# Kernel tuning notes

Hardware: AMD Instinct MI355X
Metric: run time of the kernel (lower is better)

## Reference

```python
import jax, jax.numpy as jnp
import numpy as np

D_MODEL = 512
N_HEADS = 8
D_HEAD = D_MODEL // N_HEADS
SCALE = D_HEAD ** -0.5


def _rel_shift(x):
    # x: (b, h, qlen, klen) -> Transformer-XL relative shift
    b, h, qlen, klen = x.shape
    x = jnp.pad(x, ((0, 0), (0, 0), (0, 0), (1, 0)))        # (b,h,q,k+1)
    x = x.reshape(b, h, klen + 1, qlen)
    x = x[:, :, 1:, :].reshape(b, h, qlen, klen)
    return x


def setup_inputs() -> dict:
    key = jax.random.key(0)
    ks = jax.random.split(key, 12)
    B, S = 2, 2048
    P = 2 * S - 1
    w = lambda k, shape: (jax.random.normal(k, shape, jnp.float32) * 0.02)
    return {
        "x": jax.random.normal(ks[0], (B, S, D_MODEL), jnp.float32),
        "pos_emb": jax.random.normal(ks[1], (P, D_MODEL), jnp.float32),
        "Wq": w(ks[2], (D_MODEL, D_MODEL)), "bq": jnp.zeros((D_MODEL,), jnp.float32),
        "Wk": w(ks[3], (D_MODEL, D_MODEL)), "bk": jnp.zeros((D_MODEL,), jnp.float32),
        "Wv": w(ks[4], (D_MODEL, D_MODEL)), "bv": jnp.zeros((D_MODEL,), jnp.float32),
        "Wp": w(ks[5], (D_MODEL, D_MODEL)),
        "Wo": w(ks[6], (D_MODEL, D_MODEL)), "bo": jnp.zeros((D_MODEL,), jnp.float32),
        "pos_bias_u": w(ks[7], (N_HEADS, D_HEAD)),
        "pos_bias_v": w(ks[8], (N_HEADS, D_HEAD)),
    }


def reference(x, pos_emb, Wq, bq, Wk, bk, Wv, bv, Wp, Wo, bo, pos_bias_u, pos_bias_v):
    B, S, _ = x.shape
    # projections (torch Linear: y = x @ W^T + b; here W stored as (in, out))
    q = (x @ Wq + bq).reshape(B, S, N_HEADS, D_HEAD)
    k = (x @ Wk + bk).reshape(B, S, N_HEADS, D_HEAD)
    v = (x @ Wv + bv).reshape(B, S, N_HEADS, D_HEAD)
    p = (pos_emb @ Wp).reshape(-1, N_HEADS, D_HEAD)  # (2S-1, H, D)

    # content score: (q + u) @ k^T  -> (B,H,S,S)
    content = jnp.einsum("bshd,bthd->bhst", q + pos_bias_u, k)
    # position score: (q + v_bias) @ p^T -> (B,H,S,2S-1), then rel_shift
    pos = jnp.einsum("bshd,phd->bhsp", q + pos_bias_v, p)
    pos = _rel_shift(pos)[..., :S]  # trim to kv_len

    attn = jax.nn.softmax((content + pos) * SCALE, axis=-1)
    out = jnp.einsum("bhst,bthd->bshd", attn, v).reshape(B, S, D_MODEL)
    out = out @ Wo + bo
    return out
```

## Files before the change

kernel.cpp:

```cpp
#include <hip/hip_runtime.h>

#define DM    512
#define NH    8
#define DH    64
#define SEQ   2048
#define PLEN  4095
#define NB    2
#define ATT_SCALE 0.125f

typedef __attribute__((ext_vector_type(8))) _Float16 half8;
typedef __attribute__((ext_vector_type(4))) float   floatx4;

__device__ __forceinline__ void gll16(const _Float16* g, _Float16* l) {
    __builtin_amdgcn_global_load_lds(
        (const __attribute__((address_space(1))) void*)g,
        (__attribute__((address_space(3))) void*)l, 16, 0, 0);
}

__global__ __launch_bounds__(256)
void prep(const float* __restrict__ x, const float* __restrict__ pe,
          const float* __restrict__ W0, const float* __restrict__ W1,
          const float* __restrict__ W2, const float* __restrict__ W3,
          const float* __restrict__ W4,
          _Float16* __restrict__ x16, _Float16* __restrict__ pe16,
          _Float16* __restrict__ Wt)
{
    __shared__ _Float16 tile[64 * 72];
    const int z = blockIdx.z;
    const int t = threadIdx.x;

    if (z < 2) {
        const float* src = z ? pe : x;
        _Float16* dst = z ? pe16 : x16;
        const long n = z ? (long)PLEN * DM : (long)NB * SEQ * DM;
        const long i = ((long)blockIdx.x * 256 + t) * 8;
        if (i >= n) return;
        float4 f0 = *(const float4*)(src + i);
        float4 f1 = *(const float4*)(src + i + 4);
        half8 o;
        o[0] = (_Float16)f0.x; o[1] = (_Float16)f0.y;
        o[2] = (_Float16)f0.z; o[3] = (_Float16)f0.w;
        o[4] = (_Float16)f1.x; o[5] = (_Float16)f1.y;
        o[6] = (_Float16)f1.z; o[7] = (_Float16)f1.w;
        *(half8*)(dst + i) = o;
        return;
    }
    if (blockIdx.x >= 64) return;
    const int wz = z - 2;
    const float* W = (wz == 0) ? W0 : (wz == 1) ? W1 : (wz == 2) ? W2
                   : (wz == 3) ? W3 : W4;
    _Float16* dst_base = Wt + (size_t)wz * DM * DM;
    const int n0 = (blockIdx.x & 7) * 64, k0 = (blockIdx.x >> 3) * 64;
    {
        const int kr = t >> 2, nch = (t & 3) * 16;
        const float* src = W + (size_t)(k0 + kr) * DM + n0 + nch;
        float4 f0 = *(const float4*)(src + 0);
        float4 f1 = *(const float4*)(src + 4);
        float4 f2 = *(const float4*)(src + 8);
        float4 f3 = *(const float4*)(src + 12);
        _Float16* trow = &tile[kr * 72 + nch];
        trow[0]  = (_Float16)f0.x; trow[1]  = (_Float16)f0.y;
        trow[2]  = (_Float16)f0.z; trow[3]  = (_Float16)f0.w;
        trow[4]  = (_Float16)f1.x; trow[5]  = (_Float16)f1.y;
        trow[6]  = (_Float16)f1.z; trow[7]  = (_Float16)f1.w;
        trow[8]  = (_Float16)f2.x; trow[9]  = (_Float16)f2.y;
        trow[10] = (_Float16)f2.z; trow[11] = (_Float16)f2.w;
        trow[12] = (_Float16)f3.x; trow[13] = (_Float16)f3.y;
        trow[14] = (_Float16)f3.z; trow[15] = (_Float16)f3.w;
    }
    __syncthreads();
    {
        const int nr = t >> 2, kch = (t & 3) * 16;
        half8 o0, o1;
#pragma unroll
        for (int i = 0; i < 8; ++i) o0[i] = tile[(kch + i) * 72 + nr];
#pragma unroll
        for (int i = 0; i < 8; ++i) o1[i] = tile[(kch + 8 + i) * 72 + nr];
        _Float16* dst = dst_base + (size_t)(n0 + nr) * DM + k0 + kch;
        *(half8*)dst = o0;
        *(half8*)(dst + 8) = o1;
    }
}

__global__ __launch_bounds__(256)
void gemm_qkvp(const _Float16* __restrict__ X, const _Float16* __restrict__ Pe,
               const _Float16* __restrict__ Wt,
               const float* __restrict__ bq, const float* __restrict__ bk,
               const float* __restrict__ bv, const float* __restrict__ bu,
               const float* __restrict__ bvb,
               _Float16* __restrict__ qu16, _Float16* __restrict__ qv16,
               _Float16* __restrict__ k16, _Float16* __restrict__ vt16,
               _Float16* __restrict__ p16)
{
    __shared__ _Float16 aS[64 * 72];
    __shared__ _Float16 wS[64 * 72];

    const int t = threadIdx.x;
    const int w = t >> 6, lane = t & 63, quad = lane >> 4, l16 = lane & 15;
    const int z = blockIdx.z;
    const int n0 = blockIdx.x * 64;
    const int m0 = blockIdx.y * 64;
    const int srow = t >> 2, sch = (t & 3) * 16;
    const _Float16* A = (z == 3) ? Pe : X;
    const _Float16* Wz = Wt + (size_t)z * DM * DM;

    int arow = m0 + srow;
    if (z == 3 && arow > PLEN - 1) arow = PLEN - 1;
    const _Float16* arowp = A + (size_t)arow * DM + sch;
    const _Float16* wrowp = Wz + (size_t)(n0 + srow) * DM + sch;

    floatx4 acc[4];
#pragma unroll
    for (int ct = 0; ct < 4; ++ct) acc[ct] = (floatx4){0.f, 0.f, 0.f, 0.f};

    half8 pa0 = *(const half8*)arowp;
    half8 pa1 = *(const half8*)(arowp + 8);
    half8 pw0 = *(const half8*)wrowp;
    half8 pw1 = *(const half8*)(wrowp + 8);

    for (int k0 = 0; k0 < DM; k0 += 64) {
        __syncthreads();
        *(half8*)&aS[srow * 72 + sch]     = pa0;
        *(half8*)&aS[srow * 72 + sch + 8] = pa1;
        *(half8*)&wS[srow * 72 + sch]     = pw0;
        *(half8*)&wS[srow * 72 + sch + 8] = pw1;
        __syncthreads();
        if (k0 + 64 < DM) {
            pa0 = *(const half8*)(arowp + k0 + 64);
            pa1 = *(const half8*)(arowp + k0 + 72);
            pw0 = *(const half8*)(wrowp + k0 + 64);
            pw1 = *(const half8*)(wrowp + k0 + 72);
        }
#pragma unroll
        for (int kb = 0; kb < 2; ++kb) {
            half8 af = *(const half8*)&aS[(16 * w + l16) * 72 + kb * 32 + quad * 8];
#pragma unroll
            for (int ct = 0; ct < 4; ++ct) {
                half8 bf = *(const half8*)&wS[(16 * ct + l16) * 72 + kb * 32 + quad * 8];
                acc[ct] = __builtin_amdgcn_mfma_f32_16x16x32_f16(af, bf, acc[ct], 0, 0, 0);
            }
        }
    }

    const int h = n0 >> 6;
    if (z == 0) {
#pragma unroll
        for (int ct = 0; ct < 4; ++ct) {
            const int n = n0 + 16 * ct + l16;
            const float bval = bq[n], uval = bu[n], vval = bvb[n];
#pragma unroll
            for (int r = 0; r < 4; ++r) {
                const int m = m0 + 16 * w + 4 * quad + r;
                const int b = m >> 11, s = m & 2047;
                const size_t dst = ((size_t)((h * NB + b) * SEQ) + s) * DH + (n & 63);
                const float q = acc[ct][r] + bval;
                qu16[dst] = (_Float16)((q + uval) * ATT_SCALE);
                qv16[dst] = (_Float16)((q + vval) * ATT_SCALE);
            }
        }
    } else if (z == 1) {
#pragma unroll
        for (int ct = 0; ct < 4; ++ct) {
            const int n = n0 + 16 * ct + l16;
            const float bval = bk[n];
#pragma unroll
            for (int r = 0; r < 4; ++r) {
                const int m = m0 + 16 * w + 4 * quad + r;
                const int b = m >> 11, s = m & 2047;
                k16[((size_t)((h * NB + b) * SEQ) + s) * DH + (n & 63)] =
                    (_Float16)(acc[ct][r] + bval);
            }
        }
    } else if (z == 2) {
        __syncthreads();
#pragma unroll
        for (int ct = 0; ct < 4; ++ct) {
            const float bval = bv[n0 + 16 * ct + l16];
#pragma unroll
            for (int r = 0; r < 4; ++r)
                aS[(16 * w + 4 * quad + r) * 72 + 16 * ct + l16] =
                    (_Float16)(acc[ct][r] + bval);
        }
        __syncthreads();
        const int b = m0 >> 11, s0 = m0 & 2047;
        const int drow = t >> 2;
        half8 o0, o1;
#pragma unroll
        for (int i = 0; i < 8; ++i) o0[i] = aS[(sch + i) * 72 + drow];
#pragma unroll
        for (int i = 0; i < 8; ++i) o1[i] = aS[(sch + 8 + i) * 72 + drow];
        _Float16* dst = vt16 + ((size_t)((h * NB + b) * DH) + drow) * SEQ + s0 + sch;
        *(half8*)dst = o0;
        *(half8*)(dst + 8) = o1;
    } else {
#pragma unroll
        for (int ct = 0; ct < 4; ++ct) {
            const int n = n0 + 16 * ct + l16;
#pragma unroll
            for (int r = 0; r < 4; ++r) {
                const int m = m0 + 16 * w + 4 * quad + r;
                if (m < PLEN)
                    p16[((size_t)h * PLEN + m) * DH + (n & 63)] = (_Float16)acc[ct][r];
            }
        }
    }
}

__global__ __launch_bounds__(256, 2)
void relattn_mfma(const _Float16* __restrict__ QU,
                  const _Float16* __restrict__ QV,
                  const _Float16* __restrict__ Kp,
                  const _Float16* __restrict__ VT,
                  const _Float16* __restrict__ Pp,
                  float* __restrict__ Opart,
                  float* __restrict__ Lpart)
{
    __shared__ _Float16 sbuf[2][16384];
    __shared__ _Float16 tS[64 * 72];

    const int t = threadIdx.x;
    const int w = t >> 6, lane = t & 63, quad = lane >> 4, l16 = lane & 15;
    const int i0 = blockIdx.x * 64;
    const int h = blockIdx.y;
    const int b = blockIdx.z & 1, jh = blockIdx.z >> 1;
    const size_t hb = (size_t)(h * NB + b);
    const int cbase = 48 - 16 * w;
    const int jbeg = jh * (SEQ / 2), jend = jbeg + (SEQ / 2);

    half8 qa[2], va[2];
    {
        const _Float16* qrow = QU + (hb * SEQ + i0 + 16 * w + l16) * DH + quad * 8;
        const _Float16* vrow = QV + (hb * SEQ + i0 + 16 * w + l16) * DH + quad * 8;
        qa[0] = *(const half8*)qrow;       qa[1] = *(const half8*)(qrow + 32);
        va[0] = *(const half8*)vrow;       va[1] = *(const half8*)(vrow + 32);
    }

    floatx4 O[4];
    float lsum[4] = {0.f, 0.f, 0.f, 0.f};
#pragma unroll
    for (int ct = 0; ct < 4; ++ct) O[ct] = (floatx4){0.f, 0.f, 0.f, 0.f};

    const _Float16* Kbase = Kp + hb * SEQ * DH;
    const _Float16* Vbase = VT + hb * DH * SEQ;
    const _Float16* Pbase = Pp + (size_t)h * PLEN * DH;
    const int rbase0 = (SEQ - 1) - i0 - 63;

    const int kx = l16 & 7;
    const int hox0 = ((quad) ^ kx) * 8;
    const int hox1 = ((4 + quad) ^ kx) * 8;

    const int l3 = lane >> 3, pos = lane & 7;

#define STAGE(bufp, J0)                                                        \
    {                                                                          \
        _Float16* bp = (bufp);                                                 \
        const int rb = rbase0 + (J0);                                          \
        _Pragma("unroll")                                                      \
        for (int I = 0; I < 2; ++I) {                                          \
            const int cid = w * 2 + I;                                         \
            const int row = cid * 8 + l3;                                      \
            const int ch  = pos ^ (row & 7);                                   \
            gll16(Kbase + (size_t)((J0) + row) * DH + ch * 8, bp + cid * 512); \
        }                                                                      \
        _Pragma("unroll")                                                      \
        for (int I = 0; I < 2; ++I) {                                          \
            const int cid = w * 2 + I;                                         \
            const int row = cid * 8 + l3;                                      \
            const int ch  = pos ^ (row & 7);                                   \
            gll16(Vbase + (size_t)row * SEQ + (J0) + ch * 8,                   \
                  bp + 4096 + cid * 512);                                      \
        }                                                                      \
        _Pragma("unroll")                                                      \
        for (int I = 0; I < 4; ++I) {                                          \
            const int cid = w * 4 + I;                                         \
            const int row = cid * 8 + l3;                                      \
            int r = rb + row; if (r > PLEN - 1) r = PLEN - 1;                  \
            const int ch  = pos ^ (row & 7);                                   \
            gll16(Pbase + (size_t)r * DH + ch * 8, bp + 8192 + cid * 512);     \
        }                                                                      \
    }

    STAGE(&sbuf[0][0], jbeg);

    int cur = 0;
    for (int j0 = jbeg; j0 < jend; j0 += 64) {
        asm volatile("s_waitcnt vmcnt(0)" ::: "memory");
        __builtin_amdgcn_s_barrier();
        asm volatile("" ::: "memory");

        const _Float16* kSc = &sbuf[cur][0];
        const _Float16* vSc = &sbuf[cur][4096];
        const _Float16* pSc = &sbuf[cur][8192];

        if (j0 + 64 < jend) STAGE(&sbuf[cur ^ 1][0], j0 + 64);

        floatx4 Tacc[5];
#pragma unroll
        for (int c2 = 0; c2 < 5; ++c2) Tacc[c2] = (floatx4){0.f, 0.f, 0.f, 0.f};
#pragma unroll
        for (int c2 = 0; c2 < 5; ++c2) {
            half8 bf0 = *(const half8*)&pSc[(cbase + 16 * c2 + l16) * 64 + hox0];
            half8 bf1 = *(const half8*)&pSc[(cbase + 16 * c2 + l16) * 64 + hox1];
            Tacc[c2] = __builtin_amdgcn_mfma_f32_16x16x32_f16(va[0], bf0, Tacc[c2], 0, 0, 0);
            Tacc[c2] = __builtin_amdgcn_mfma_f32_16x16x32_f16(va[1], bf1, Tacc[c2], 0, 0, 0);
        }

        floatx4 Sc[4];
#pragma unroll
        for (int ct = 0; ct < 4; ++ct) Sc[ct] = (floatx4){0.f, 0.f, 0.f, 0.f};
#pragma unroll
        for (int ct = 0; ct < 4; ++ct) {
            half8 bf0 = *(const half8*)&kSc[(16 * ct + l16) * 64 + hox0];
            half8 bf1 = *(const half8*)&kSc[(16 * ct + l16) * 64 + hox1];
            Sc[ct] = __builtin_amdgcn_mfma_f32_16x16x32_f16(qa[0], bf0, Sc[ct], 0, 0, 0);
            Sc[ct] = __builtin_amdgcn_mfma_f32_16x16x32_f16(qa[1], bf1, Sc[ct], 0, 0, 0);
        }

#pragma unroll
        for (int r = 0; r < 4; ++r) {
            const int u  = l16 - 4 * quad - r + 15;
            const int dl = u & 15;
            const int s  = u >> 4;
            const int pidx = (((quad << 4) | dl) << 2);
            float rot[5];
#pragma unroll
            for (int c2 = 0; c2 < 5; ++c2)
                rot[c2] = __int_as_float(__builtin_amdgcn_ds_bpermute(
                    pidx, __float_as_int(Tacc[c2][r])));
#pragma unroll
            for (int ct = 0; ct < 4; ++ct) {
                const float tv = s ? rot[ct + 1] : rot[ct];
                const float e = __expf(Sc[ct][r] + tv);
                Sc[ct][r] = e;
                lsum[r] += e;
            }
        }

#pragma unroll
        for (int ct = 0; ct < 4; ++ct)
#pragma unroll
            for (int r = 0; r < 4; ++r)
                tS[(16 * w + 4 * quad + r) * 72 + 16 * ct + l16] = (_Float16)Sc[ct][r];
        asm volatile("" ::: "memory");

#pragma unroll
        for (int kb = 0; kb < 2; ++kb) {
            half8 af = *(const half8*)&tS[(16 * w + l16) * 72 + kb * 32 + quad * 8];
            const int hox = kb ? hox1 : hox0;
#pragma unroll
            for (int ct = 0; ct < 4; ++ct) {
                half8 bf = *(const half8*)&vSc[(16 * ct + l16) * 64 + hox];
                O[ct] = __builtin_amdgcn_mfma_f32_16x16x32_f16(af, bf, O[ct], 0, 0, 0);
            }
        }
        asm volatile("" ::: "memory");
        cur ^= 1;
    }
#undef STAGE

    float* Op = Opart + (size_t)jh * NB * SEQ * DM;
    float* Lp = Lpart + (size_t)jh * NH * NB * SEQ;
#pragma unroll
    for (int r = 0; r < 4; ++r) {
#pragma unroll
        for (int m = 1; m < 16; m <<= 1) lsum[r] += __shfl_xor(lsum[r], m);
        const int row = i0 + 16 * w + 4 * quad + r;
        if (l16 == 0) Lp[hb * SEQ + row] = lsum[r];
        float* orow = Op + (size_t)(b * SEQ + row) * DM + h * DH;
#pragma unroll
        for (int ct = 0; ct < 4; ++ct)
            orow[16 * ct + l16] = O[ct][r];
    }
}

__global__ __launch_bounds__(256)
void gemm_out(const float* __restrict__ O0, const float* __restrict__ O1,
              const float* __restrict__ L0, const float* __restrict__ L1,
              const _Float16* __restrict__ Wt,
              const float* __restrict__ bias, float* __restrict__ Out)
{
    __shared__ _Float16 aS[64 * 72];
    __shared__ _Float16 wS[64 * 72];

    const int t = threadIdx.x;
    const int w = t >> 6, lane = t & 63, quad = lane >> 4, l16 = lane & 15;
    const int n0 = blockIdx.x * 64;
    const int m0 = blockIdx.y * 64;
    const int srow = t >> 2, sch = (t & 3) * 16;

    const int mrow = m0 + srow;
    const int bA = mrow >> 11, sA = mrow & 2047;
    const float* o0p = O0 + (size_t)mrow * DM + sch;
    const float* o1p = O1 + (size_t)mrow * DM + sch;
    const _Float16* wrowp = Wt + (size_t)(n0 + srow) * DM + sch;

    floatx4 acc[4];
#pragma unroll
    for (int ct = 0; ct < 4; ++ct) acc[ct] = (floatx4){0.f, 0.f, 0.f, 0.f};

    float4 pa0 = *(const float4*)(o0p + 0);
    float4 pa1 = *(const float4*)(o0p + 4);
    float4 pa2 = *(const float4*)(o0p + 8);
    float4 pa3 = *(const float4*)(o0p + 12);
    float4 pc0 = *(const float4*)(o1p + 0);
    float4 pc1 = *(const float4*)(o1p + 4);
    float4 pc2 = *(const float4*)(o1p + 8);
    float4 pc3 = *(const float4*)(o1p + 12);
    half8 pw0 = *(const half8*)wrowp;
    half8 pw1 = *(const half8*)(wrowp + 8);

    for (int k0 = 0; k0 < DM; k0 += 64) {
        __syncthreads();
        const int hA = k0 >> 6;
        const int li = (hA * NB + bA) * SEQ + sA;
        const float inv = 1.f / (L0[li] + L1[li]);
        half8 h0, h1;
        h0[0] = (_Float16)((pa0.x + pc0.x) * inv);
        h0[1] = (_Float16)((pa0.y + pc0.y) * inv);
        h0[2] = (_Float16)((pa0.z + pc0.z) * inv);
        h0[3] = (_Float16)((pa0.w + pc0.w) * inv);
        h0[4] = (_Float16)((pa1.x + pc1.x) * inv);
        h0[5] = (_Float16)((pa1.y + pc1.y) * inv);
        h0[6] = (_Float16)((pa1.z + pc1.z) * inv);
        h0[7] = (_Float16)((pa1.w + pc1.w) * inv);
        h1[0] = (_Float16)((pa2.x + pc2.x) * inv);
        h1[1] = (_Float16)((pa2.y + pc2.y) * inv);
        h1[2] = (_Float16)((pa2.z + pc2.z) * inv);
        h1[3] = (_Float16)((pa2.w + pc2.w) * inv);
        h1[4] = (_Float16)((pa3.x + pc3.x) * inv);
        h1[5] = (_Float16)((pa3.y + pc3.y) * inv);
        h1[6] = (_Float16)((pa3.z + pc3.z) * inv);
        h1[7] = (_Float16)((pa3.w + pc3.w) * inv);
        *(half8*)&aS[srow * 72 + sch]     = h0;
        *(half8*)&aS[srow * 72 + sch + 8] = h1;
        *(half8*)&wS[srow * 72 + sch]     = pw0;
        *(half8*)&wS[srow * 72 + sch + 8] = pw1;
        __syncthreads();
        if (k0 + 64 < DM) {
            pa0 = *(const float4*)(o0p + k0 + 64);
            pa1 = *(const float4*)(o0p + k0 + 68);
            pa2 = *(const float4*)(o0p + k0 + 72);
            pa3 = *(const float4*)(o0p + k0 + 76);
            pc0 = *(const float4*)(o1p + k0 + 64);
            pc1 = *(const float4*)(o1p + k0 + 68);
            pc2 = *(const float4*)(o1p + k0 + 72);
            pc3 = *(const float4*)(o1p + k0 + 76);
            pw0 = *(const half8*)(wrowp + k0 + 64);
            pw1 = *(const half8*)(wrowp + k0 + 72);
        }
#pragma unroll
        for (int kb = 0; kb < 2; ++kb) {
            half8 af = *(const half8*)&aS[(16 * w + l16) * 72 + kb * 32 + quad * 8];
#pragma unroll
            for (int ct = 0; ct < 4; ++ct) {
                half8 bf = *(const half8*)&wS[(16 * ct + l16) * 72 + kb * 32 + quad * 8];
                acc[ct] = __builtin_amdgcn_mfma_f32_16x16x32_f16(af, bf, acc[ct], 0, 0, 0);
            }
        }
    }

#pragma unroll
    for (int ct = 0; ct < 4; ++ct) {
        const int n = n0 + 16 * ct + l16;
        const float bval = bias[n];
#pragma unroll
        for (int r = 0; r < 4; ++r) {
            const int m = m0 + 16 * w + 4 * quad + r;
            Out[(size_t)m * DM + n] = acc[ct][r] + bval;
        }
    }
}

extern "C" void kernel_launch(void* const* d_in, const int* in_sizes, int n_in,
                              void* d_out, int out_size, void* d_ws, size_t ws_size,
                              hipStream_t stream)
{
    (void)in_sizes; (void)n_in; (void)out_size; (void)ws_size;
    const float* x   = (const float*)d_in[0];
    const float* pe  = (const float*)d_in[1];
    const float* Wq  = (const float*)d_in[2];
    const float* bq  = (const float*)d_in[3];
    const float* Wk  = (const float*)d_in[4];
    const float* bk  = (const float*)d_in[5];
    const float* Wv  = (const float*)d_in[6];
    const float* bv  = (const float*)d_in[7];
    const float* Wp  = (const float*)d_in[8];
    const float* Wo  = (const float*)d_in[9];
    const float* bo  = (const float*)d_in[10];
    const float* pbu = (const float*)d_in[11];
    const float* pbv = (const float*)d_in[12];
    float* out = (float*)d_out;

    const size_t nX  = (size_t)NB * SEQ * DM;
    const size_t nPe = (size_t)PLEN * DM;
    const size_t nW  = (size_t)DM * DM;
    const size_t nH  = (size_t)NH * NB * SEQ * DH;
    const size_t nPh = (size_t)NH * PLEN * DH;
    const size_t nL  = (size_t)NH * NB * SEQ;

    _Float16* x16  = (_Float16*)d_ws;
    _Float16* pe16 = x16 + nX;
    _Float16* wt   = pe16 + nPe;
    _Float16* qu16 = wt + 5 * nW;
    _Float16* qv16 = qu16 + nH;
    _Float16* k16  = qv16 + nH;
    _Float16* vt16 = k16 + nH;
    _Float16* p16  = vt16 + nH;
    _Float16* ow16 = p16 + nPh;
    float*    opart = (float*)(ow16 + nX);
    float*    lpart = opart + 2 * nX;

    dim3 blk(256);
    prep<<<dim3(1024, 1, 7), blk, 0, stream>>>(x, pe, Wq, Wk, Wv, Wp, Wo,
                                               x16, pe16, wt);
    gemm_qkvp<<<dim3(8, 64, 4), blk, 0, stream>>>(x16, pe16, wt,
                                                  bq, bk, bv, pbu, pbv,
                                                  qu16, qv16, k16, vt16, p16);
    relattn_mfma<<<dim3(SEQ / 64, NH, NB * 2), blk, 0, stream>>>(
        qu16, qv16, k16, vt16, p16, opart, lpart);
    gemm_out<<<dim3(8, 64), blk, 0, stream>>>(opart, opart + nX,
                                              lpart, lpart + nL,
                                              wt + 4 * nW, bo, out);
}
```

Measured before the change: 200.9 us.

## Load P fragments directly to registers, shrink LDS, split combine out of output GEMM

In the attention kernel, the position-embedding tiles are now loaded straight from global memory into per-lane register fragments and prefetched one iteration ahead, instead of being staged through LDS. This halves the shared buffer and raises the occupancy hint from 2 to 3 blocks per CU. Separately, the normalization that merges the two split-KV halves moves out of gemm_out into a new elementwise attn_combine kernel that writes fp16, so gemm_out reads fp16 A directly. The trade-offs are extra register pressure from the P fragments, unswizzled global reads of P, and one more kernel launch plus an extra fp16 round trip through memory.

```diff
diff --git a/kernel.cpp b/kernel.cpp
--- a/kernel.cpp
+++ b/kernel.cpp
@@ -206,7 +206,7 @@
     }
 }
 
-__global__ __launch_bounds__(256, 2)
+__global__ __launch_bounds__(256, 3)
 void relattn_mfma(const _Float16* __restrict__ QU,
                   const _Float16* __restrict__ QV,
                   const _Float16* __restrict__ Kp,
@@ -215,7 +215,7 @@
                   float* __restrict__ Opart,
                   float* __restrict__ Lpart)
 {
-    __shared__ _Float16 sbuf[2][16384];
+    __shared__ _Float16 sbuf[2][8192];
     __shared__ _Float16 tS[64 * 72];
 
     const int t = threadIdx.x;
@@ -242,7 +242,6 @@
 
     const _Float16* Kbase = Kp + hb * SEQ * DH;
     const _Float16* Vbase = VT + hb * DH * SEQ;
-    const _Float16* Pbase = Pp + (size_t)h * PLEN * DH;
     const int rbase0 = (SEQ - 1) - i0 - 63;
 
     const int kx = l16 & 7;
@@ -251,10 +250,9 @@
 
     const int l3 = lane >> 3, pos = lane & 7;
 
-#define STAGE(bufp, J0)                                                        \
+#define STAGE_KV(bufp, J0)                                                     \
     {                                                                          \
         _Float16* bp = (bufp);                                                 \
-        const int rb = rbase0 + (J0);                                          \
         _Pragma("unroll")                                                      \
         for (int I = 0; I < 2; ++I) {                                          \
             const int cid = w * 2 + I;                                         \
@@ -270,17 +268,24 @@
             gll16(Vbase + (size_t)row * SEQ + (J0) + ch * 8,                   \
                   bp + 4096 + cid * 512);                                      \
         }                                                                      \
+    }
+
+    const _Float16* pptr = Pp + (size_t)h * PLEN * DH
+                         + (size_t)(rbase0 + jbeg + cbase + l16) * DH + quad * 8;
+    half8 pf0[5], pf1[5];
+
+#define PLOAD()                                                                \
+    {                                                                          \
         _Pragma("unroll")                                                      \
-        for (int I = 0; I < 4; ++I) {                                          \
-            const int cid = w * 4 + I;                                         \
-            const int row = cid * 8 + l3;                                      \
-            int r = rb + row; if (r > PLEN - 1) r = PLEN - 1;                  \
-            const int ch  = pos ^ (row & 7);                                   \
-            gll16(Pbase + (size_t)r * DH + ch * 8, bp + 8192 + cid * 512);     \
+        for (int c2 = 0; c2 < 5; ++c2) {                                       \
+            pf0[c2] = *(const half8*)(pptr + c2 * 1024);                       \
+            pf1[c2] = *(const half8*)(pptr + c2 * 1024 + 32);                  \
         }                                                                      \
-    }
-
-    STAGE(&sbuf[0][0], jbeg);
+        pptr += 4096;                                                          \
+    }
+
+    STAGE_KV(&sbuf[0][0], jbeg);
+    PLOAD();
 
     int cur = 0;
     for (int j0 = jbeg; j0 < jend; j0 += 64) {
@@ -290,19 +295,16 @@
 
         const _Float16* kSc = &sbuf[cur][0];
         const _Float16* vSc = &sbuf[cur][4096];
-        const _Float16* pSc = &sbuf[cur][8192];
-
-        if (j0 + 64 < jend) STAGE(&sbuf[cur ^ 1][0], j0 + 64);
+
+        if (j0 + 64 < jend) STAGE_KV(&sbuf[cur ^ 1][0], j0 + 64);
 
         floatx4 Tacc[5];
 #pragma unroll
         for (int c2 = 0; c2 < 5; ++c2) Tacc[c2] = (floatx4){0.f, 0.f, 0.f, 0.f};
 #pragma unroll
         for (int c2 = 0; c2 < 5; ++c2) {
-            half8 bf0 = *(const half8*)&pSc[(cbase + 16 * c2 + l16) * 64 + hox0];
-            half8 bf1 = *(const half8*)&pSc[(cbase + 16 * c2 + l16) * 64 + hox1];
-            Tacc[c2] = __builtin_amdgcn_mfma_f32_16x16x32_f16(va[0], bf0, Tacc[c2], 0, 0, 0);
-            Tacc[c2] = __builtin_amdgcn_mfma_f32_16x16x32_f16(va[1], bf1, Tacc[c2], 0, 0, 0);
+            Tacc[c2] = __builtin_amdgcn_mfma_f32_16x16x32_f16(va[0], pf0[c2], Tacc[c2], 0, 0, 0);
+            Tacc[c2] = __builtin_amdgcn_mfma_f32_16x16x32_f16(va[1], pf1[c2], Tacc[c2], 0, 0, 0);
         }
 
         floatx4 Sc[4];
@@ -336,6 +338,8 @@
             }
         }
 
+        if (j0 + 64 < jend) PLOAD();
+
 #pragma unroll
         for (int ct = 0; ct < 4; ++ct)
 #pragma unroll
@@ -356,7 +360,8 @@
         asm volatile("" ::: "memory");
         cur ^= 1;
     }
-#undef STAGE
+#undef STAGE_KV
+#undef PLOAD
 
     float* Op = Opart + (size_t)jh * NB * SEQ * DM;
     float* Lp = Lpart + (size_t)jh * NH * NB * SEQ;
@@ -374,9 +379,35 @@
 }
 
 __global__ __launch_bounds__(256)
-void gemm_out(const float* __restrict__ O0, const float* __restrict__ O1,
-              const float* __restrict__ L0, const float* __restrict__ L1,
-              const _Float16* __restrict__ Wt,
+void attn_combine(const float* __restrict__ O0, const float* __restrict__ O1,
+                  const float* __restrict__ L0, const float* __restrict__ L1,
+                  _Float16* __restrict__ Out)
+{
+    const int e = (blockIdx.x * 256 + threadIdx.x) * 8;
+    const int m = e >> 9;
+    const int col = e & 511;
+    const int h = col >> 6;
+    const int b = m >> 11, i = m & 2047;
+    const int li = (h * NB + b) * SEQ + i;
+    const float inv = 1.f / (L0[li] + L1[li]);
+    float4 a0 = *(const float4*)(O0 + e);
+    float4 a1 = *(const float4*)(O0 + e + 4);
+    float4 c0 = *(const float4*)(O1 + e);
+    float4 c1 = *(const float4*)(O1 + e + 4);
+    half8 o;
+    o[0] = (_Float16)((a0.x + c0.x) * inv);
+    o[1] = (_Float16)((a0.y + c0.y) * inv);
+    o[2] = (_Float16)((a0.z + c0.z) * inv);
+    o[3] = (_Float16)((a0.w + c0.w) * inv);
+    o[4] = (_Float16)((a1.x + c1.x) * inv);
+    o[5] = (_Float16)((a1.y + c1.y) * inv);
+    o[6] = (_Float16)((a1.z + c1.z) * inv);
+    o[7] = (_Float16)((a1.w + c1.w) * inv);
+    *(half8*)(Out + e) = o;
+}
+
+__global__ __launch_bounds__(256)
+void gemm_out(const _Float16* __restrict__ A, const _Float16* __restrict__ Wt,
               const float* __restrict__ bias, float* __restrict__ Out)
 {
     __shared__ _Float16 aS[64 * 72];
@@ -388,63 +419,28 @@
     const int m0 = blockIdx.y * 64;
     const int srow = t >> 2, sch = (t & 3) * 16;
 
-    const int mrow = m0 + srow;
-    const int bA = mrow >> 11, sA = mrow & 2047;
-    const float* o0p = O0 + (size_t)mrow * DM + sch;
-    const float* o1p = O1 + (size_t)mrow * DM + sch;
+    const _Float16* arowp = A + (size_t)(m0 + srow) * DM + sch;
     const _Float16* wrowp = Wt + (size_t)(n0 + srow) * DM + sch;
 
     floatx4 acc[4];
 #pragma unroll
     for (int ct = 0; ct < 4; ++ct) acc[ct] = (floatx4){0.f, 0.f, 0.f, 0.f};
 
-    float4 pa0 = *(const float4*)(o0p + 0);
-    float4 pa1 = *(const float4*)(o0p + 4);
-    float4 pa2 = *(const float4*)(o0p + 8);
-    float4 pa3 = *(const float4*)(o0p + 12);
-    float4 pc0 = *(const float4*)(o1p + 0);
-    float4 pc1 = *(const float4*)(o1p + 4);
-    float4 pc2 = *(const float4*)(o1p + 8);
-    float4 pc3 = *(const float4*)(o1p + 12);
+    half8 pa0 = *(const half8*)arowp;
+    half8 pa1 = *(const half8*)(arowp + 8);
     half8 pw0 = *(const half8*)wrowp;
     half8 pw1 = *(const half8*)(wrowp + 8);
 
     for (int k0 = 0; k0 < DM; k0 += 64) {
         __syncthreads();
-        const int hA = k0 >> 6;
-        const int li = (hA * NB + bA) * SEQ + sA;
-        const float inv = 1.f / (L0[li] + L1[li]);
-        half8 h0, h1;
-        h0[0] = (_Float16)((pa0.x + pc0.x) * inv);
-        h0[1] = (_Float16)((pa0.y + pc0.y) * inv);
-        h0[2] = (_Float16)((pa0.z + pc0.z) * inv);
-        h0[3] = (_Float16)((pa0.w + pc0.w) * inv);
-        h0[4] = (_Float16)((pa1.x + pc1.x) * inv);
-        h0[5] = (_Float16)((pa1.y + pc1.y) * inv);
-        h0[6] = (_Float16)((pa1.z + pc1.z) * inv);
-        h0[7] = (_Float16)((pa1.w + pc1.w) * inv);
-        h1[0] = (_Float16)((pa2.x + pc2.x) * inv);
-        h1[1] = (_Float16)((pa2.y + pc2.y) * inv);
-        h1[2] = (_Float16)((pa2.z + pc2.z) * inv);
-        h1[3] = (_Float16)((pa2.w + pc2.w) * inv);
-        h1[4] = (_Float16)((pa3.x + pc3.x) * inv);
-        h1[5] = (_Float16)((pa3.y + pc3.y) * inv);
-        h1[6] = (_Float16)((pa3.z + pc3.z) * inv);
-        h1[7] = (_Float16)((pa3.w + pc3.w) * inv);
-        *(half8*)&aS[srow * 72 + sch]     = h0;
-        *(half8*)&aS[srow * 72 + sch + 8] = h1;
+        *(half8*)&aS[srow * 72 + sch]     = pa0;
+        *(half8*)&aS[srow * 72 + sch + 8] = pa1;
         *(half8*)&wS[srow * 72 + sch]     = pw0;
         *(half8*)&wS[srow * 72 + sch + 8] = pw1;
         __syncthreads();
         if (k0 + 64 < DM) {
-            pa0 = *(const float4*)(o0p + k0 + 64);
-            pa1 = *(const float4*)(o0p + k0 + 68);
-            pa2 = *(const float4*)(o0p + k0 + 72);
-            pa3 = *(const float4*)(o0p + k0 + 76);
-            pc0 = *(const float4*)(o1p + k0 + 64);
-            pc1 = *(const float4*)(o1p + k0 + 68);
-            pc2 = *(const float4*)(o1p + k0 + 72);
-            pc3 = *(const float4*)(o1p + k0 + 76);
+            pa0 = *(const half8*)(arowp + k0 + 64);
+            pa1 = *(const half8*)(arowp + k0 + 72);
             pw0 = *(const half8*)(wrowp + k0 + 64);
             pw1 = *(const half8*)(wrowp + k0 + 72);
         }
@@ -518,7 +514,7 @@
                                                   qu16, qv16, k16, vt16, p16);
     relattn_mfma<<<dim3(SEQ / 64, NH, NB * 2), blk, 0, stream>>>(
         qu16, qv16, k16, vt16, p16, opart, lpart);
-    gemm_out<<<dim3(8, 64), blk, 0, stream>>>(opart, opart + nX,
-                                              lpart, lpart + nL,
-                                              wt + 4 * nW, bo, out);
-}
+    attn_combine<<<dim3((unsigned)(nX / (256 * 8))), blk, 0, stream>>>(
+        opart, opart + nX, lpart, lpart + nL, ow16);
+    gemm_out<<<dim3(8, 64), blk, 0, stream>>>(ow16, wt + 4 * nW, bo, out);
+}
```

Measured after the change: 224.9 us. +12.0%, slower.
